# Optimization experiments

Measured on AMD Instinct MI355X. Metric: run time of the kernel, lower is better.

## Reference

```python
import jax, jax.numpy as jnp
import numpy as np

B, L, D = 4, 4096, 1024
H = 16
DK = D // H  # 64
EPS = 1e-5


def setup_inputs() -> dict:
    key = jax.random.key(0)
    ks = jax.random.split(key, 9)
    s = 1.0 / np.sqrt(D)
    return {
        "Q": jax.random.normal(ks[0], (B, L, D), dtype=jnp.float32),
        "W_Q": jax.random.uniform(ks[1], (D, D), jnp.float32, -s, s),
        "b_Q": jax.random.uniform(ks[2], (D,), jnp.float32, -s, s),
        "W_K": jax.random.uniform(ks[3], (D, D), jnp.float32, -s, s),
        "b_K": jax.random.uniform(ks[4], (D,), jnp.float32, -s, s),
        "W_V": jax.random.uniform(ks[5], (D, D), jnp.float32, -s, s),
        "b_V": jax.random.uniform(ks[6], (D,), jnp.float32, -s, s),
        "W_O": jax.random.uniform(ks[7], (D, D), jnp.float32, -s, s),
        "b_O": jax.random.uniform(ks[8], (D,), jnp.float32, -s, s),
    }


def reference(Q, W_Q, b_Q, W_K, b_K, W_V, b_V, W_O, b_O):
    # Projections (torch Linear: x @ W.T + b). K = V = Q (self-attention).
    q = (Q @ W_Q.T + b_Q).reshape(B, L, H, DK)  # blhd
    k = (Q @ W_K.T + b_K).reshape(B, L, H, DK)
    v = (Q @ W_V.T + b_V).reshape(B, L, H, DK)

    phi_q = jax.nn.elu(q) + 1.0
    phi_k = jax.nn.elu(k) + 1.0

    # KV outer-product accumulation over sequence: [b,h,d,m]
    KV = jnp.einsum('blhd,blhm->bhdm', phi_k, v)
    K_sum = phi_k.sum(axis=1)                       # [b,h,d]
    Z = 1.0 / (jnp.einsum('blhd,bhd->blh', phi_q, K_sum) + EPS)
    V_new = jnp.einsum('blhd,bhdm->blhm', phi_q, KV) * Z[..., None]

    out = V_new.reshape(B, L, H * DK) @ W_O.T + b_O  # [b,L,d_model]
    return out
```

## Files before the change

### kernel.cpp

```cpp
#include <hip/hip_runtime.h>

typedef unsigned short u16;
typedef unsigned int   u32;
typedef __attribute__((ext_vector_type(8))) short short8;
typedef __attribute__((ext_vector_type(4))) float f32x4;
typedef __attribute__((ext_vector_type(4))) u16   u16x4;

#define NB 4
#define SL 4096
#define DM 1024
#define NH 16
#define DK 64

__device__ __forceinline__ u16 f2bf(float f) {
  u32 u = __builtin_bit_cast(u32, f);
  u = (u + 0x7fffu + ((u >> 16) & 1u)) >> 16;
  return (u16)u;
}
__device__ __forceinline__ float bf2f(u16 v) {
  u32 u = ((u32)v) << 16;
  return __builtin_bit_cast(float, u);
}
__device__ __forceinline__ float eluP1(float x) {
  return x > 0.f ? x + 1.f : __expf(x);
}
#define GLL(gp, lp) __builtin_amdgcn_global_load_lds(     \
    (const __attribute__((address_space(1))) void*)(gp),  \
    (__attribute__((address_space(3))) void*)(lp), 16, 0, 0)

__global__ void cvt_all(const float* __restrict__ Qf,
                        const float* __restrict__ WQ, const float* __restrict__ WK,
                        const float* __restrict__ WV, const float* __restrict__ WO,
                        const float* __restrict__ bQ, const float* __restrict__ bK,
                        const float* __restrict__ bV,
                        u16* __restrict__ Qbf, u16* __restrict__ Wqkv,
                        u16* __restrict__ Wobf, float* __restrict__ biasQKV) {
  int b = blockIdx.x, tid = threadIdx.x;
  if (b < 16384) {
    int i = b * 256 + tid;
    f32x4 f = *(const f32x4*)(Qf + (size_t)i * 4);
    u16x4 o = { f2bf(f[0]), f2bf(f[1]), f2bf(f[2]), f2bf(f[3]) };
    *(u16x4*)(Qbf + (size_t)i * 4) = o;
  } else if (b < 20480) {
    int r = (b - 16384) >> 10;
    int i = ((b - 16384) & 1023) * 256 + tid;
    const float* src = r == 0 ? WQ : r == 1 ? WK : r == 2 ? WV : WO;
    u16* dst = (r == 3) ? Wobf : Wqkv + (size_t)r * 1048576;
    f32x4 f = *(const f32x4*)(src + (size_t)i * 4);
    u16x4 o = { f2bf(f[0]), f2bf(f[1]), f2bf(f[2]), f2bf(f[3]) };
    *(u16x4*)(dst + (size_t)i * 4) = o;
  } else {
    int i = (b - 20480) * 256 + tid;
    if (i < 3072) {
      float v = (i < 1024) ? bQ[i] : (i < 2048) ? bK[i - 1024] : bV[i - 2048];
      biasQKV[i] = v;
    }
  }
}


#define VM6 asm volatile("s_waitcnt vmcnt(6)" ::: "memory")
#define NOP ((void)0)

#define SA(buf, ks, kt) do {                                      \
    const u16* g_ = Ag + (((kt) & 15) * 64 + (ks) * 32);          \
    u16* l_ = ldsA + (buf) * 32768 + (ks) * 8192;                 \
    GLL(g_, l_); GLL(g_ + 16 * 1024, l_ + 512); } while (0)

#define SB(buf, ks, kt) do {                                      \
    const u16* g_ = Wg + (((kt) & 15) * 64 + (ks) * 32);          \
    u16* l_ = ldsB + (buf) * 32768 + (ks) * 8192;                 \
    GLL(g_, l_); GLL(g_ + 16 * 1024, l_ + 512); } while (0)

#define LDB(buf, ks) do {                                         \
    const u16* pB_ = bBase + (buf) * 32768 + (ks) * 8192;         \
    bf0 = *(const short8*)(pB_ + bOff[0]);                        \
    bf1 = *(const short8*)(pB_ + bOff[1]);                        \
    bf2 = *(const short8*)(pB_ + bOff[2]);                        \
    bf3 = *(const short8*)(pB_ + bOff[3]); } while (0)

#define PHASE(buf, ks, tb, PRE, STG, WT) do {                     \
    short8 af_[4];                                                \
    const u16* pA_ = aBase + (buf) * 32768 + (ks) * 8192;         \
    _Pragma("unroll") for (int t_ = 0; t_ < 4; t_++)              \
      af_[t_] = *(const short8*)(pA_ + aOff[(tb) + t_]);          \
    PRE;                                                          \
    STG;                                                          \
    WT;                                                           \
    __builtin_amdgcn_s_barrier();                                 \
    asm volatile("s_waitcnt lgkmcnt(0)" ::: "memory");            \
    __builtin_amdgcn_s_setprio(1);                                \
    _Pragma("unroll") for (int t_ = 0; t_ < 4; t_++) {            \
      acc[(tb) + t_][0] = __builtin_amdgcn_mfma_f32_16x16x32_bf16(af_[t_], bf0, acc[(tb) + t_][0], 0, 0, 0); \
      acc[(tb) + t_][1] = __builtin_amdgcn_mfma_f32_16x16x32_bf16(af_[t_], bf1, acc[(tb) + t_][1], 0, 0, 0); \
      acc[(tb) + t_][2] = __builtin_amdgcn_mfma_f32_16x16x32_bf16(af_[t_], bf2, acc[(tb) + t_][2], 0, 0, 0); \
      acc[(tb) + t_][3] = __builtin_amdgcn_mfma_f32_16x16x32_bf16(af_[t_], bf3, acc[(tb) + t_][3], 0, 0, 0); \
    }                                                             \
    __builtin_amdgcn_s_setprio(0);                                \
    __builtin_amdgcn_s_barrier();                                 \
  } while (0)

__global__ __launch_bounds__(512, 2) void gemm_qkv(const u16* __restrict__ A,
                                                   const u16* __restrict__ Wqkv,
                                                   const float* __restrict__ biasQKV,
                                                   u16* __restrict__ phiq,
                                                   u16* __restrict__ phiKT,
                                                   u16* __restrict__ vT) {
  const int K = 1024;
  const int bId = blockIdx.x;
  const int xcd = bId & 7, s = bId >> 3;
  const int tile_m = xcd * 8 + s / 12;
  const int tile_n = s % 12;
  const int region = tile_n >> 2;

  const int tid = threadIdx.x, lane = tid & 63, wv = tid >> 6;
  const int i16 = lane & 15, q = lane >> 4;
  const int waveM = wv >> 2, waveN = wv & 3;

  __shared__ u16 smem[65536];

  const int r0 = wv * 32 + (lane >> 2);
  const int kc = (lane & 3) ^ ((r0 >> 1) & 3);
  const u16* Ag = A + (size_t)(tile_m * 256 + r0) * K + kc * 8;
  const u16* Wg = Wqkv + (size_t)(tile_n * 256 + r0) * K + kc * 8;
  u16* ldsA = smem + wv * 1024;
  u16* ldsB = smem + 16384 + wv * 1024;

  const u16* aBase = (region == 0) ? smem + 16384 : smem;
  const u16* bBase = (region == 0) ? smem : smem + 16384;
  int aOff[8], bOff[4];
#pragma unroll
  for (int t = 0; t < 8; t++) {
    int m = waveM * 128 + t * 16 + i16;
    aOff[t] = m * 32 + ((q ^ ((m >> 1) & 3)) << 3);
  }
#pragma unroll
  for (int u = 0; u < 4; u++) {
    int n = waveN * 64 + u * 16 + i16;
    bOff[u] = n * 32 + ((q ^ ((n >> 1) & 3)) << 3);
  }

  f32x4 acc[8][4] = {};
  short8 bf0, bf1, bf2, bf3;

  SB(0, 0, 0); SA(0, 0, 0); SB(0, 1, 0); SA(0, 1, 0);
  SB(1, 0, 1); SA(1, 0, 1); SB(1, 1, 1);
  VM6;
  __builtin_amdgcn_s_barrier();
  asm volatile("" ::: "memory");

#pragma unroll 1
  for (int i = 0; i < 8; i++) {
    PHASE(0, 0, 0, LDB(0, 0), SA(1, 1, 2 * i + 1), NOP);
    PHASE(0, 0, 4, NOP,       SB(0, 0, 2 * i + 2), NOP);
    PHASE(0, 1, 0, LDB(0, 1), SA(0, 0, 2 * i + 2), NOP);
    PHASE(0, 1, 4, NOP,       SB(0, 1, 2 * i + 2), VM6);
    PHASE(1, 0, 0, LDB(1, 0), SA(0, 1, 2 * i + 2), NOP);
    PHASE(1, 0, 4, NOP,       SB(1, 0, 2 * i + 3), NOP);
    PHASE(1, 1, 0, LDB(1, 1), SA(1, 0, 2 * i + 3), NOP);
    PHASE(1, 1, 4, NOP,       SB(1, 1, 2 * i + 3), VM6);
  }

  u16* T = smem;
  const int TS = 132;
  u16* dstT = (region == 1) ? phiKT : vT;
  const int bI = tile_m >> 4;
  const int lb = (tile_m & 15) * 256;

#pragma unroll
  for (int h = 0; h < 2; h++) {
    __syncthreads();
    if (waveM == h) {
      if (region == 0) {
#pragma unroll
        for (int t = 0; t < 8; t++) {
          f32x4 b4 = *(const f32x4*)(biasQKV + tile_n * 256 + h * 128 + t * 16 + q * 4);
#pragma unroll
          for (int u = 0; u < 4; u++) {
            int cC = waveN * 64 + u * 16 + i16;
            u16x4 o;
#pragma unroll
            for (int r = 0; r < 4; r++) o[r] = f2bf(eluP1(acc[t][u][r] + b4[r]));
            *(u16x4*)(T + cC * TS + t * 16 + q * 4) = o;
          }
        }
      } else {
#pragma unroll
        for (int u = 0; u < 4; u++) {
          int cC = waveN * 64 + u * 16 + i16;
          float bs = biasQKV[tile_n * 256 + cC];
#pragma unroll
          for (int t = 0; t < 8; t++) {
            u16x4 o;
#pragma unroll
            for (int r = 0; r < 4; r++) {
              float vv = acc[t][u][r] + bs;
              if (region == 1) vv = eluP1(vv);
              o[r] = f2bf(vv);
            }
            *(u16x4*)(T + cC * TS + t * 16 + q * 4) = o;
          }
        }
      }
    }
    __syncthreads();
    {
      const int Rl = tid >> 4, c16 = (tid & 15) * 8;
#pragma unroll
      for (int p = 0; p < 8; p++) {
        int R = p * 32 + Rl;
        short8 v8 = *(const short8*)(T + R * TS + c16);
        if (region == 0) {
          *(short8*)(phiq + (size_t)(tile_m * 256 + R) * DM + tile_n * 256 + h * 128 + c16) = v8;
        } else {
          int n_loc = tile_n * 256 + R - region * 1024;
          *(short8*)(dstT + ((size_t)bI * 1024 + n_loc) * 4096 + lb + h * 128 + c16) = v8;
        }
      }
    }
  }
}

#define COMPUTE(CB)                                                          \
  do {                                                                       \
    short8 af_[4], bf_[4];                                                   \
    _Pragma("unroll") for (int t = 0; t < 4; t++)                            \
        af_[t] = *(const short8*)(aP[t] + (CB));                             \
    _Pragma("unroll") for (int u = 0; u < 4; u++)                            \
        bf_[u] = *(const short8*)(bP[u] + (CB));                             \
    _Pragma("unroll") for (int t = 0; t < 4; t++)                            \
      _Pragma("unroll") for (int u = 0; u < 4; u++)                          \
          acc[t][u] = __builtin_amdgcn_mfma_f32_16x16x32_bf16(               \
              af_[t], bf_[u], acc[t][u], 0, 0, 0);                           \
  } while (0)

#define STAGE4(XB, WB)                                        \
  do {                                                        \
    GLL(Ag0, XB); GLL(Ag1, (XB) + 512);                       \
    GLL(Wg0, WB); GLL(Wg1, (WB) + 512);                       \
    Ag0 += 32; Ag1 += 32; Wg0 += 32; Wg1 += 32;               \
  } while (0)

__global__ __launch_bounds__(256) void gemm_out(const u16* __restrict__ A,
                                                const u16* __restrict__ W,
                                                const float* __restrict__ bias,
                                                float* __restrict__ outp) {
  const int K = 1024;
  const int bId = blockIdx.x;
  const int xcd = bId & 7, s = bId >> 3;
  const int xm = xcd >> 1, xn = xcd & 1;
  const int tm_l = s >> 2, tn_l = s & 3;
  const int tile_m = xm * 32 + tm_l;
  const int tile_n = xn * 4 + tn_l;

  const int tid = threadIdx.x, lane = tid & 63, wv = tid >> 6;
  const int i16 = lane & 15, q = lane >> 4;
  const int waveR = wv >> 1, waveC = wv & 1;

  __shared__ u16 smem[17408];

  const int rbase = wv * 32 + (lane >> 2);
  const int kc = (lane & 3) ^ ((rbase >> 1) & 3);
  const u16* Ag0 = A + (size_t)(tile_m * 128 + rbase) * K + kc * 8;
  const u16* Ag1 = Ag0 + 16 * K;
  const u16* Wg0 = W + (size_t)(tile_n * 128 + rbase) * K + kc * 8;
  const u16* Wg1 = Wg0 + 16 * K;
  u16* X0 = smem + wv * 1024;
  u16* W0 = smem + 4096 + wv * 1024;
  u16* X1 = X0 + 8192;
  u16* W1 = W0 + 8192;

  const u16* aP[4];
  const u16* bP[4];
#pragma unroll
  for (int t = 0; t < 4; t++) {
    int m = waveR * 64 + t * 16 + i16;
    aP[t] = smem + 4096 + m * 32 + ((q ^ ((m >> 1) & 3)) << 3);
  }
#pragma unroll
  for (int u = 0; u < 4; u++) {
    int m = waveC * 64 + u * 16 + i16;
    bP[u] = smem + m * 32 + ((q ^ ((m >> 1) & 3)) << 3);
  }

  f32x4 acc[4][4] = {};

  STAGE4(X0, W0);

  for (int kk = 0; kk < 16; kk++) {
    __syncthreads();
    STAGE4(X1, W1);
    COMPUTE(0);
    __syncthreads();
    if (kk < 15) STAGE4(X0, W0);
    COMPUTE(8192);
  }

  float* Tf = (float*)smem;
#pragma unroll
  for (int half = 0; half < 2; half++) {
    __syncthreads();
    if (waveR == half) {
#pragma unroll
      for (int t = 0; t < 4; t++) {
#pragma unroll
        for (int u = 0; u < 4; u++) {
          int cI = waveC * 64 + u * 16 + i16;
          int rIh = t * 16 + q * 4;
          f32x4 b4 = *(const f32x4*)(bias + tile_n * 128 + half * 64 + rIh);
          f32x4 o;
#pragma unroll
          for (int r = 0; r < 4; r++) o[r] = acc[t][u][r] + b4[r];
          *(f32x4*)(Tf + cI * 68 + rIh) = o;
        }
      }
    }
    __syncthreads();
    const int Rl = tid >> 4, j = tid & 15;
#pragma unroll
    for (int p = 0; p < 8; p++) {
      int R = p * 16 + Rl;
      f32x4 v = *(const f32x4*)(Tf + R * 68 + j * 4);
      *(f32x4*)(outp + (size_t)(tile_m * 128 + R) * DM + tile_n * 128 + half * 64 + j * 4) = v;
    }
  }
}

__global__ __launch_bounds__(256) void kv_partial(const u16* __restrict__ phiKT,
                                                  const u16* __restrict__ vT,
                                                  float* __restrict__ part,
                                                  float* __restrict__ ksumP) {
  int bh = blockIdx.x >> 2, chunk = blockIdx.x & 3;
  int tid = threadIdx.x, lane = tid & 63, wv = tid >> 6;
  int i16 = lane & 15, q = lane >> 4;
  const u16* Ab = phiKT + (size_t)bh * DK * SL;
  const u16* Bb = vT + (size_t)bh * DK * SL;
  int l0 = (chunk * 4 + wv) * 256;
  f32x4 acc[4][4] = {};
  float ks[4] = {};
  for (int kk = 0; kk < 256; kk += 32) {
    int col = l0 + kk + q * 8;
    short8 af[4], bfr[4];
#pragma unroll
    for (int t = 0; t < 4; t++) af[t] = *(const short8*)(Ab + (size_t)(t * 16 + i16) * SL + col);
#pragma unroll
    for (int u = 0; u < 4; u++) bfr[u] = *(const short8*)(Bb + (size_t)(u * 16 + i16) * SL + col);
#pragma unroll
    for (int t = 0; t < 4; t++)
#pragma unroll
      for (int j = 0; j < 8; j++) ks[t] += bf2f((u16)af[t][j]);
#pragma unroll
    for (int t = 0; t < 4; t++)
#pragma unroll
      for (int u = 0; u < 4; u++)
        acc[t][u] = __builtin_amdgcn_mfma_f32_16x16x32_bf16(af[t], bfr[u], acc[t][u], 0, 0, 0);
  }
  __shared__ float red[4][64][64];
  __shared__ float ksl[4][4][64];
#pragma unroll
  for (int t = 0; t < 4; t++)
#pragma unroll
    for (int u = 0; u < 4; u++)
#pragma unroll
      for (int r = 0; r < 4; r++)
        red[wv][t * 16 + q * 4 + r][u * 16 + i16] = acc[t][u][r];
#pragma unroll
  for (int t = 0; t < 4; t++) ksl[wv][q][t * 16 + i16] = ks[t];
  __syncthreads();
  int d = tid >> 2, mg = (tid & 3) * 16;
#pragma unroll
  for (int c = 0; c < 4; c++) {
    int m = mg + c * 4;
    f32x4 o;
#pragma unroll
    for (int r = 0; r < 4; r++)
      o[r] = red[0][d][m + r] + red[1][d][m + r] + red[2][d][m + r] + red[3][d][m + r];
    *(f32x4*)(part + ((size_t)(chunk * 64 + bh) * 64 + d) * 64 + m) = o;
  }
  if (tid < 64) {
    float s = 0.f;
#pragma unroll
    for (int w2 = 0; w2 < 4; w2++)
#pragma unroll
      for (int q2 = 0; q2 < 4; q2++) s += ksl[w2][q2][tid];
    ksumP[chunk * 4096 + bh * 64 + tid] = s;
  }
}

__global__ __launch_bounds__(256) void kv_finalize(const float* __restrict__ part,
                                                   const float* __restrict__ ksumP,
                                                   u16* __restrict__ KVt,
                                                   float* __restrict__ Ksum) {
  int bh = blockIdx.x, tid = threadIdx.x;
  for (int e = tid; e < 4096; e += 256) {
    int d = e >> 6, m = e & 63;
    float s = part[((size_t)(0 * 64 + bh) * 64 + d) * 64 + m]
            + part[((size_t)(1 * 64 + bh) * 64 + d) * 64 + m]
            + part[((size_t)(2 * 64 + bh) * 64 + d) * 64 + m]
            + part[((size_t)(3 * 64 + bh) * 64 + d) * 64 + m];
    KVt[(size_t)bh * 4096 + m * 64 + d] = f2bf(s);
  }
  if (tid < 64) {
    float s = ksumP[0 * 4096 + bh * 64 + tid] + ksumP[1 * 4096 + bh * 64 + tid]
            + ksumP[2 * 4096 + bh * 64 + tid] + ksumP[3 * 4096 + bh * 64 + tid];
    Ksum[bh * 64 + tid] = s;
  }
}

__global__ __launch_bounds__(256) void vnew_kernel(const u16* __restrict__ phiq,
                                                   const u16* __restrict__ KVt,
                                                   const float* __restrict__ Ksum,
                                                   u16* __restrict__ Vnew) {
  int bh = blockIdx.x >> 5, lt = blockIdx.x & 31;
  int b = bh >> 4, h = bh & 15;
  int tid = threadIdx.x, lane = tid & 63, wv = tid >> 6;
  int i16 = lane & 15, q = lane >> 4;
  int waveM = wv & 1, waveL = wv >> 1;

  __shared__ float Zs[128];
  __shared__ float Pp[128][2];
  __shared__ u16 T[128 * 72];
  {
    int l = tid >> 1, half = tid & 1;
    const u16* pr = phiq + (size_t)(b * SL + lt * 128 + l) * DM + h * 64 + half * 32;
    float s = 0.f;
    for (int i = 0; i < 32; i += 8) {
      short8 v8 = *(const short8*)(pr + i);
#pragma unroll
      for (int j = 0; j < 8; j++) s += bf2f((u16)v8[j]) * Ksum[bh * 64 + half * 32 + i + j];
    }
    Pp[l][half] = s;
  }
  __syncthreads();
  if (tid < 128) Zs[tid] = 1.0f / (Pp[tid][0] + Pp[tid][1] + 1e-5f);
  __syncthreads();

  f32x4 acc[2][4] = {};
#pragma unroll
  for (int step = 0; step < 2; step++) {
    int d0 = step * 32 + q * 8;
    short8 af[2], bfr[4];
#pragma unroll
    for (int t = 0; t < 2; t++) {
      int m = waveM * 32 + t * 16 + i16;
      af[t] = *(const short8*)(KVt + (size_t)bh * 4096 + m * 64 + d0);
    }
#pragma unroll
    for (int u = 0; u < 4; u++) {
      int l = lt * 128 + waveL * 64 + u * 16 + i16;
      bfr[u] = *(const short8*)(phiq + (size_t)(b * SL + l) * DM + h * 64 + d0);
    }
#pragma unroll
    for (int t = 0; t < 2; t++)
#pragma unroll
      for (int u = 0; u < 4; u++)
        acc[t][u] = __builtin_amdgcn_mfma_f32_16x16x32_bf16(af[t], bfr[u], acc[t][u], 0, 0, 0);
  }

#pragma unroll
  for (int t = 0; t < 2; t++) {
#pragma unroll
    for (int u = 0; u < 4; u++) {
      int cI = waveL * 64 + u * 16 + i16;
      int nI = waveM * 32 + t * 16 + q * 4;
      float z = Zs[cI];
      u16x4 o;
#pragma unroll
      for (int r = 0; r < 4; r++) o[r] = f2bf(acc[t][u][r] * z);
      *(u16x4*)(T + cI * 72 + nI) = o;
    }
  }
  __syncthreads();
  {
    const int Rl = tid >> 3, j = tid & 7;
#pragma unroll
    for (int p = 0; p < 4; p++) {
      int R = p * 32 + Rl;
      short8 v8 = *(const short8*)(T + R * 72 + j * 8);
      *(short8*)(Vnew + (size_t)(b * SL + lt * 128 + R) * DM + h * 64 + j * 8) = v8;
    }
  }
}

extern "C" void kernel_launch(void* const* d_in, const int* in_sizes, int n_in,
                              void* d_out, int out_size, void* d_ws, size_t ws_size,
                              hipStream_t stream) {
  const float* Qf = (const float*)d_in[0];
  const float* WQ = (const float*)d_in[1];
  const float* bQ = (const float*)d_in[2];
  const float* WK = (const float*)d_in[3];
  const float* bK = (const float*)d_in[4];
  const float* WV = (const float*)d_in[5];
  const float* bV = (const float*)d_in[6];
  const float* WO = (const float*)d_in[7];
  const float* bO = (const float*)d_in[8];

  const size_t MB = 1024ull * 1024ull;
  char* ws = (char*)d_ws;
  u16* Qbf     = (u16*)(ws + 0);
  u16* Vnew    = (u16*)(ws + 0);
  u16* Wqkv    = (u16*)(ws + 32 * MB);
  u16* Wobf    = (u16*)(ws + 38 * MB);
  float* biasQKV = (float*)(ws + 40 * MB);
  u16* phiq    = (u16*)(ws + 41 * MB);
  u16* phiKT   = (u16*)(ws + 73 * MB);
  u16* vT      = (u16*)(ws + 105 * MB);
  u16* KVt     = (u16*)(ws + 137 * MB);
  float* Ksum  = (float*)(ws + 138 * MB);
  float* part  = (float*)(ws + 139 * MB);
  float* ksumP = (float*)(ws + 143 * MB);

  cvt_all<<<20492, 256, 0, stream>>>(Qf, WQ, WK, WV, WO, bQ, bK, bV,
                                     Qbf, Wqkv, Wobf, biasQKV);

  gemm_qkv<<<768, 512, 0, stream>>>(Qbf, Wqkv, biasQKV, phiq, phiKT, vT);

  kv_partial<<<256, 256, 0, stream>>>(phiKT, vT, part, ksumP);
  kv_finalize<<<64, 256, 0, stream>>>(part, ksumP, KVt, Ksum);

  vnew_kernel<<<2048, 256, 0, stream>>>(phiq, KVt, Ksum, Vnew);

  gemm_out<<<1024, 256, 0, stream>>>(Vnew, Wobf, bO, (float*)d_out);
}
```

Before: 344.7 us.

## Reuse 256x256 pipelined GEMM for output projection and fuse normalizer into vnew

Replaces the 128x128 double-buffered output-projection GEMM with the same 256x256, 512-thread, 8-phase pipelined main loop used by the QKV GEMM, launching 256 blocks instead of 1024. This gives more reuse per tile and a deeper load/compute overlap. In vnew_kernel, the normalizer dot product phi_q·Ksum is now computed from the MFMA operand registers and reduced with lane shuffles, which removes a separate global reread of phi_q and two block barriers. The risk is that only 256 large blocks run, which may leave some CUs underused, and the epilogue becomes longer.

```diff
diff --git a/kernel.cpp b/kernel.cpp
--- a/kernel.cpp
+++ b/kernel.cpp
@@ -100,6 +100,24 @@
     __builtin_amdgcn_s_barrier();                                 \
   } while (0)
 
+#define MAIN_8PHASE_LOOP                                          \
+  SB(0, 0, 0); SA(0, 0, 0); SB(0, 1, 0); SA(0, 1, 0);             \
+  SB(1, 0, 1); SA(1, 0, 1); SB(1, 1, 1);                          \
+  VM6;                                                            \
+  __builtin_amdgcn_s_barrier();                                   \
+  asm volatile("" ::: "memory");                                  \
+  _Pragma("unroll 1")                                             \
+  for (int i = 0; i < 8; i++) {                                   \
+    PHASE(0, 0, 0, LDB(0, 0), SA(1, 1, 2 * i + 1), NOP);          \
+    PHASE(0, 0, 4, NOP,       SB(0, 0, 2 * i + 2), NOP);          \
+    PHASE(0, 1, 0, LDB(0, 1), SA(0, 0, 2 * i + 2), NOP);          \
+    PHASE(0, 1, 4, NOP,       SB(0, 1, 2 * i + 2), VM6);          \
+    PHASE(1, 0, 0, LDB(1, 0), SA(0, 1, 2 * i + 2), NOP);          \
+    PHASE(1, 0, 4, NOP,       SB(1, 0, 2 * i + 3), NOP);          \
+    PHASE(1, 1, 0, LDB(1, 1), SA(1, 0, 2 * i + 3), NOP);          \
+    PHASE(1, 1, 4, NOP,       SB(1, 1, 2 * i + 3), VM6);          \
+  }
+
 __global__ __launch_bounds__(512, 2) void gemm_qkv(const u16* __restrict__ A,
                                                    const u16* __restrict__ Wqkv,
                                                    const float* __restrict__ biasQKV,
@@ -143,23 +161,7 @@
   f32x4 acc[8][4] = {};
   short8 bf0, bf1, bf2, bf3;
 
-  SB(0, 0, 0); SA(0, 0, 0); SB(0, 1, 0); SA(0, 1, 0);
-  SB(1, 0, 1); SA(1, 0, 1); SB(1, 1, 1);
-  VM6;
-  __builtin_amdgcn_s_barrier();
-  asm volatile("" ::: "memory");
-
-#pragma unroll 1
-  for (int i = 0; i < 8; i++) {
-    PHASE(0, 0, 0, LDB(0, 0), SA(1, 1, 2 * i + 1), NOP);
-    PHASE(0, 0, 4, NOP,       SB(0, 0, 2 * i + 2), NOP);
-    PHASE(0, 1, 0, LDB(0, 1), SA(0, 0, 2 * i + 2), NOP);
-    PHASE(0, 1, 4, NOP,       SB(0, 1, 2 * i + 2), VM6);
-    PHASE(1, 0, 0, LDB(1, 0), SA(0, 1, 2 * i + 2), NOP);
-    PHASE(1, 0, 4, NOP,       SB(1, 0, 2 * i + 3), NOP);
-    PHASE(1, 1, 0, LDB(1, 1), SA(1, 0, 2 * i + 3), NOP);
-    PHASE(1, 1, 4, NOP,       SB(1, 1, 2 * i + 3), VM6);
-  }
+  MAIN_8PHASE_LOOP
 
   u16* T = smem;
   const int TS = 132;
@@ -221,107 +223,77 @@
   }
 }
 
-#define COMPUTE(CB)                                                          \
-  do {                                                                       \
-    short8 af_[4], bf_[4];                                                   \
-    _Pragma("unroll") for (int t = 0; t < 4; t++)                            \
-        af_[t] = *(const short8*)(aP[t] + (CB));                             \
-    _Pragma("unroll") for (int u = 0; u < 4; u++)                            \
-        bf_[u] = *(const short8*)(bP[u] + (CB));                             \
-    _Pragma("unroll") for (int t = 0; t < 4; t++)                            \
-      _Pragma("unroll") for (int u = 0; u < 4; u++)                          \
-          acc[t][u] = __builtin_amdgcn_mfma_f32_16x16x32_bf16(               \
-              af_[t], bf_[u], acc[t][u], 0, 0, 0);                           \
-  } while (0)
-
-#define STAGE4(XB, WB)                                        \
-  do {                                                        \
-    GLL(Ag0, XB); GLL(Ag1, (XB) + 512);                       \
-    GLL(Wg0, WB); GLL(Wg1, (WB) + 512);                       \
-    Ag0 += 32; Ag1 += 32; Wg0 += 32; Wg1 += 32;               \
-  } while (0)
-
-__global__ __launch_bounds__(256) void gemm_out(const u16* __restrict__ A,
-                                                const u16* __restrict__ W,
-                                                const float* __restrict__ bias,
-                                                float* __restrict__ outp) {
+__global__ __launch_bounds__(512, 2) void gemm_out(const u16* __restrict__ A,
+                                                   const u16* __restrict__ W,
+                                                   const float* __restrict__ bias,
+                                                   float* __restrict__ outp) {
   const int K = 1024;
   const int bId = blockIdx.x;
   const int xcd = bId & 7, s = bId >> 3;
-  const int xm = xcd >> 1, xn = xcd & 1;
-  const int tm_l = s >> 2, tn_l = s & 3;
-  const int tile_m = xm * 32 + tm_l;
-  const int tile_n = xn * 4 + tn_l;
+  const int tile_m = xcd * 8 + (s >> 2);
+  const int tile_n = s & 3;
 
   const int tid = threadIdx.x, lane = tid & 63, wv = tid >> 6;
   const int i16 = lane & 15, q = lane >> 4;
-  const int waveR = wv >> 1, waveC = wv & 1;
-
-  __shared__ u16 smem[17408];
-
-  const int rbase = wv * 32 + (lane >> 2);
-  const int kc = (lane & 3) ^ ((rbase >> 1) & 3);
-  const u16* Ag0 = A + (size_t)(tile_m * 128 + rbase) * K + kc * 8;
-  const u16* Ag1 = Ag0 + 16 * K;
-  const u16* Wg0 = W + (size_t)(tile_n * 128 + rbase) * K + kc * 8;
-  const u16* Wg1 = Wg0 + 16 * K;
-  u16* X0 = smem + wv * 1024;
-  u16* W0 = smem + 4096 + wv * 1024;
-  u16* X1 = X0 + 8192;
-  u16* W1 = W0 + 8192;
-
-  const u16* aP[4];
-  const u16* bP[4];
-#pragma unroll
-  for (int t = 0; t < 4; t++) {
-    int m = waveR * 64 + t * 16 + i16;
-    aP[t] = smem + 4096 + m * 32 + ((q ^ ((m >> 1) & 3)) << 3);
+  const int waveM = wv >> 2, waveN = wv & 3;
+
+  __shared__ u16 smem[65536];
+
+  const int r0 = wv * 32 + (lane >> 2);
+  const int kc = (lane & 3) ^ ((r0 >> 1) & 3);
+  const u16* Ag = A + (size_t)(tile_m * 256 + r0) * K + kc * 8;
+  const u16* Wg = W + (size_t)(tile_n * 256 + r0) * K + kc * 8;
+  u16* ldsA = smem + wv * 1024;
+  u16* ldsB = smem + 16384 + wv * 1024;
+
+  const u16* aBase = smem + 16384;
+  const u16* bBase = smem;
+  int aOff[8], bOff[4];
+#pragma unroll
+  for (int t = 0; t < 8; t++) {
+    int m = waveM * 128 + t * 16 + i16;
+    aOff[t] = m * 32 + ((q ^ ((m >> 1) & 3)) << 3);
   }
 #pragma unroll
   for (int u = 0; u < 4; u++) {
-    int m = waveC * 64 + u * 16 + i16;
-    bP[u] = smem + m * 32 + ((q ^ ((m >> 1) & 3)) << 3);
-  }
-
-  f32x4 acc[4][4] = {};
-
-  STAGE4(X0, W0);
-
-  for (int kk = 0; kk < 16; kk++) {
+    int n = waveN * 64 + u * 16 + i16;
+    bOff[u] = n * 32 + ((q ^ ((n >> 1) & 3)) << 3);
+  }
+
+  f32x4 acc[8][4] = {};
+  short8 bf0, bf1, bf2, bf3;
+
+  MAIN_8PHASE_LOOP
+
+  float* Tf = (float*)smem;
+  const int TFS = 68;
+#pragma unroll
+  for (int qn = 0; qn < 4; qn++) {
     __syncthreads();
-    STAGE4(X1, W1);
-    COMPUTE(0);
-    __syncthreads();
-    if (kk < 15) STAGE4(X0, W0);
-    COMPUTE(8192);
-  }
-
-  float* Tf = (float*)smem;
-#pragma unroll
-  for (int half = 0; half < 2; half++) {
-    __syncthreads();
-    if (waveR == half) {
-#pragma unroll
-      for (int t = 0; t < 4; t++) {
+    if (waveM == (qn >> 1)) {
+      const int tb = (qn & 1) * 4;
+#pragma unroll
+      for (int tt = 0; tt < 4; tt++) {
+        f32x4 b4 = *(const f32x4*)(bias + tile_n * 256 + qn * 64 + tt * 16 + q * 4);
 #pragma unroll
         for (int u = 0; u < 4; u++) {
-          int cI = waveC * 64 + u * 16 + i16;
-          int rIh = t * 16 + q * 4;
-          f32x4 b4 = *(const f32x4*)(bias + tile_n * 128 + half * 64 + rIh);
+          int l = waveN * 64 + u * 16 + i16;
           f32x4 o;
 #pragma unroll
-          for (int r = 0; r < 4; r++) o[r] = acc[t][u][r] + b4[r];
-          *(f32x4*)(Tf + cI * 68 + rIh) = o;
+          for (int r = 0; r < 4; r++) o[r] = acc[tb + tt][u][r] + b4[r];
+          *(f32x4*)(Tf + l * TFS + tt * 16 + q * 4) = o;
         }
       }
     }
     __syncthreads();
-    const int Rl = tid >> 4, j = tid & 15;
-#pragma unroll
-    for (int p = 0; p < 8; p++) {
-      int R = p * 16 + Rl;
-      f32x4 v = *(const f32x4*)(Tf + R * 68 + j * 4);
-      *(f32x4*)(outp + (size_t)(tile_m * 128 + R) * DM + tile_n * 128 + half * 64 + j * 4) = v;
+    {
+      const int Rl = tid >> 4, j = tid & 15;
+#pragma unroll
+      for (int p = 0; p < 8; p++) {
+        int R = p * 32 + Rl;
+        f32x4 v = *(const f32x4*)(Tf + R * TFS + j * 4);
+        *(f32x4*)(outp + (size_t)(tile_m * 256 + R) * DM + tile_n * 256 + qn * 64 + j * 4) = v;
+      }
     }
   }
 }
@@ -417,25 +389,15 @@
   int i16 = lane & 15, q = lane >> 4;
   int waveM = wv & 1, waveL = wv >> 1;
 
-  __shared__ float Zs[128];
-  __shared__ float Pp[128][2];
   __shared__ u16 T[128 * 72];
-  {
-    int l = tid >> 1, half = tid & 1;
-    const u16* pr = phiq + (size_t)(b * SL + lt * 128 + l) * DM + h * 64 + half * 32;
-    float s = 0.f;
-    for (int i = 0; i < 32; i += 8) {
-      short8 v8 = *(const short8*)(pr + i);
-#pragma unroll
-      for (int j = 0; j < 8; j++) s += bf2f((u16)v8[j]) * Ksum[bh * 64 + half * 32 + i + j];
-    }
-    Pp[l][half] = s;
-  }
-  __syncthreads();
-  if (tid < 128) Zs[tid] = 1.0f / (Pp[tid][0] + Pp[tid][1] + 1e-5f);
-  __syncthreads();
+
+  f32x4 ks00 = *(const f32x4*)(Ksum + bh * 64 + q * 8);
+  f32x4 ks01 = *(const f32x4*)(Ksum + bh * 64 + q * 8 + 4);
+  f32x4 ks10 = *(const f32x4*)(Ksum + bh * 64 + 32 + q * 8);
+  f32x4 ks11 = *(const f32x4*)(Ksum + bh * 64 + 32 + q * 8 + 4);
 
   f32x4 acc[2][4] = {};
+  float zp[4] = {0.f, 0.f, 0.f, 0.f};
 #pragma unroll
   for (int step = 0; step < 2; step++) {
     int d0 = step * 32 + q * 8;
@@ -449,12 +411,27 @@
     for (int u = 0; u < 4; u++) {
       int l = lt * 128 + waveL * 64 + u * 16 + i16;
       bfr[u] = *(const short8*)(phiq + (size_t)(b * SL + l) * DM + h * 64 + d0);
+      f32x4 k0 = step == 0 ? ks00 : ks10;
+      f32x4 k1 = step == 0 ? ks01 : ks11;
+#pragma unroll
+      for (int j = 0; j < 4; j++) zp[u] += bf2f((u16)bfr[u][j]) * k0[j];
+#pragma unroll
+      for (int j = 0; j < 4; j++) zp[u] += bf2f((u16)bfr[u][4 + j]) * k1[j];
     }
 #pragma unroll
     for (int t = 0; t < 2; t++)
 #pragma unroll
       for (int u = 0; u < 4; u++)
         acc[t][u] = __builtin_amdgcn_mfma_f32_16x16x32_bf16(af[t], bfr[u], acc[t][u], 0, 0, 0);
+  }
+
+  float z[4];
+#pragma unroll
+  for (int u = 0; u < 4; u++) {
+    float s = zp[u];
+    s += __shfl_xor(s, 16);
+    s += __shfl_xor(s, 32);
+    z[u] = 1.0f / (s + 1e-5f);
   }
 
 #pragma unroll
@@ -463,10 +440,9 @@
     for (int u = 0; u < 4; u++) {
       int cI = waveL * 64 + u * 16 + i16;
       int nI = waveM * 32 + t * 16 + q * 4;
-      float z = Zs[cI];
       u16x4 o;
 #pragma unroll
-      for (int r = 0; r < 4; r++) o[r] = f2bf(acc[t][u][r] * z);
+      for (int r = 0; r < 4; r++) o[r] = f2bf(acc[t][u][r] * z[u]);
       *(u16x4*)(T + cI * 72 + nI) = o;
     }
   }
@@ -520,5 +496,5 @@
 
   vnew_kernel<<<2048, 256, 0, stream>>>(phiq, KVt, Ksum, Vnew);
 
-  gemm_out<<<1024, 256, 0, stream>>>(Vnew, Wobf, bO, (float*)d_out);
-}
+  gemm_out<<<256, 512, 0, stream>>>(Vnew, Wobf, bO, (float*)d_out);
+}
```

New measurement: 330.1 us. 4.2% less time.
